# Optimization experiments

Hardware: AMD Instinct MI355X
Metric: run time of the kernel (lower is better)

Reference implementation:

```python
import jax, jax.numpy as jnp
import numpy as np

B, L, C, H, W = 4, 5, 64, 128, 256
VOXEL = 0.4          # args['voxel_size'][0]
DOWNSAMPLE = 2       # args['downsample_rate']


def setup_inputs() -> dict:
    key = jax.random.key(0)
    k1, k2, k3 = jax.random.split(key, 3)
    record_len = jnp.array([3, 5, 4, 4], dtype=jnp.int32)  # sum = 16
    n_tot = 16
    x = jax.random.normal(k1, (n_tot, C, H, W), dtype=jnp.float32)
    # near-identity SE(2)-ish 4x4 transforms so warps stay mostly in-bounds
    eye = jnp.eye(4, dtype=jnp.float32)
    t = jnp.broadcast_to(eye, (B, L, L, 4, 4)).copy()
    rot = jax.random.normal(k2, (B, L, L, 2, 2), dtype=jnp.float32) * 0.02
    trans = jax.random.normal(k3, (B, L, L, 2), dtype=jnp.float32) * 5.0  # meters
    t = t.at[..., :2, :2].add(rot)
    t = t.at[..., 0, 3].set(trans[..., 0])
    t = t.at[..., 1, 3].set(trans[..., 1])
    return {"x": x, "record_len": record_len, "pairwise_t_matrix": t}


def _normalize_t(t):
    # t: (B,L,L,4,4) -> normalized 2x3 affine (matches the torch in-place edits)
    m = t[..., jnp.array([0, 1]), :][..., jnp.array([0, 1, 3])]  # (B,L,L,2,3)
    m = m.at[..., 0, 1].multiply(H / W)
    m = m.at[..., 1, 0].multiply(W / H)
    m = m.at[..., 0, 2].multiply(2.0 / (DOWNSAMPLE * VOXEL * W))
    m = m.at[..., 1, 2].multiply(2.0 / (DOWNSAMPLE * VOXEL * H))
    return m


def _grid_sample(img, grid):
    # img (N,C,H,W), grid (N,H,W,2) xy in [-1,1]; bilinear, zeros padding,
    # align_corners=True (matches torch warp_affine_simple / F.grid_sample)
    n, c, h, w = img.shape
    ix = (grid[..., 0] + 1.0) * 0.5 * (w - 1)
    iy = (grid[..., 1] + 1.0) * 0.5 * (h - 1)
    x0 = jnp.floor(ix); y0 = jnp.floor(iy)
    x1 = x0 + 1.0;      y1 = y0 + 1.0
    wx1 = ix - x0; wx0 = 1.0 - wx1
    wy1 = iy - y0; wy0 = 1.0 - wy1

    def corner(xc, yc, wgt):
        valid = (xc >= 0) & (xc <= w - 1) & (yc >= 0) & (yc <= h - 1)
        xi = jnp.clip(xc, 0, w - 1).astype(jnp.int32)
        yi = jnp.clip(yc, 0, h - 1).astype(jnp.int32)
        vals = jax.vmap(lambda im, yy, xx: im[:, yy, xx])(img, yi, xi)  # (N,C,H,W)
        return vals * (wgt * valid)[:, None, :, :]

    return (corner(x0, y0, wx0 * wy0) + corner(x1, y0, wx1 * wy0)
            + corner(x0, y1, wx0 * wy1) + corner(x1, y1, wx1 * wy1))


def _fuse(x, record_len, pairwise_t_matrix):
    m = _normalize_t(pairwise_t_matrix)          # (B,L,L,2,3)
    theta = m[:, 0]                              # ego row i=0 -> (B,L,2,3)
    # affine_grid, align_corners=True: base grid over [-1,1]
    xs = jnp.linspace(-1.0, 1.0, W)
    ys = jnp.linspace(-1.0, 1.0, H)
    gx, gy = jnp.meshgrid(xs, ys)                # (H,W)
    coords = jnp.stack([gx, gy, jnp.ones_like(gx)], axis=-1)  # (H,W,3)
    grid = jnp.einsum('blij,hwj->blhwi', theta, coords)        # (B,L,H,W,2)
    # pad ragged groups to (B,L,...) via gather
    csum = jnp.cumsum(record_len)
    offsets = jnp.concatenate([jnp.zeros((1,), csum.dtype), csum[:-1]])
    idx = jnp.clip(offsets[:, None] + jnp.arange(L)[None, :], 0, x.shape[0] - 1)
    xp = x[idx]                                  # (B,L,C,H,W)
    warped = _grid_sample(xp.reshape(B * L, C, H, W),
                          grid.reshape(B * L, H, W, 2)).reshape(B, L, C, H, W)
    mask = jnp.arange(L)[None, :] < record_len[:, None]        # (B,L)
    neg_inf = jnp.array(-jnp.inf, dtype=warped.dtype)
    masked = jnp.where(mask[:, :, None, None, None], warped, neg_inf)
    return jnp.max(masked, axis=1)               # (B,C,H,W)


def reference(x, record_len, pairwise_t_matrix):
    return _fuse(x, record_len, pairwise_t_matrix)
```

## Files before the change

### kernel.cpp

```cpp
#include <hip/hip_runtime.h>
#include <math.h>

#define BB 4
#define LL 5
#define CC 64
#define HH 128
#define WW 256
#define NTOT 16
#define CG 8
#define HW (HH * WW)
#define NXCD 8
#define NWG (BB * (CC / CG) * HH)

__global__ __launch_bounds__(256) void maxfusion_kernel(
    const float* __restrict__ x,
    const int* __restrict__ record_len,
    const float* __restrict__ t,
    float* __restrict__ out)
{
    const int bid = (blockIdx.x % NXCD) * (NWG / NXCD) + blockIdx.x / NXCD;

    const int h   = bid % HH;
    const int tmp = bid / HH;
    const int cg  = tmp % (CC / CG);
    const int b   = tmp / (CC / CG);
    const int w   = threadIdx.x;

    const int rl = record_len[b];
    int off = 0;
    #pragma unroll
    for (int i = 0; i < BB; ++i) off += (i < b) ? record_len[i] : 0;

    const float gx = -1.0f + 2.0f * (float)w / (float)(WW - 1);
    const float gy = -1.0f + 2.0f * (float)h / (float)(HH - 1);

    float maxv[CG];
    #pragma unroll
    for (int c = 0; c < CG; ++c) maxv[c] = -INFINITY;

    for (int l = 0; l < rl; ++l) {
        const float* tm = t + (size_t)((b * LL * LL + l) * 16);
        const float m00 = tm[0];
        const float m01 = tm[1] * ((float)HH / (float)WW);
        const float m02 = tm[3] * (2.0f / (0.8f * (float)WW));
        const float m10 = tm[4] * ((float)WW / (float)HH);
        const float m11 = tm[5];
        const float m12 = tm[7] * (2.0f / (0.8f * (float)HH));
        const float sx  = 0.5f * (float)(WW - 1);
        const float sy  = 0.5f * (float)(HH - 1);
        const float a00 = m00 * sx, a01 = m01 * sx, a02 = (m02 + 1.0f) * sx;
        const float a10 = m10 * sy, a11 = m11 * sy, a12 = (m12 + 1.0f) * sy;

        const float ix = a00 * gx + a01 * gy + a02;
        const float iy = a10 * gx + a11 * gy + a12;

        const float x0f = floorf(ix), y0f = floorf(iy);
        const float wx1 = ix - x0f, wx0 = 1.0f - wx1;
        const float wy1 = iy - y0f, wy0 = 1.0f - wy1;
        const int x0 = (int)x0f, y0 = (int)y0f;

        const bool inx = (x0 >= 0) && (x0 <= WW - 2);
        const float wxa = inx ? wx0 : ((x0 == -1)     ? wx1 : 0.0f);
        const float wxb = inx ? wx1 : ((x0 == WW - 1) ? wx0 : 0.0f);
        const float wy0v = ((y0 >= 0)     && (y0 <= HH - 1))     ? wy0 : 0.0f;
        const float wy1v = ((y0 + 1 >= 0) && (y0 + 1 <= HH - 1)) ? wy1 : 0.0f;

        const int k  = min(max(x0, 0), WW - 2);
        const int r0 = min(max(y0,     0), HH - 1);
        const int r1 = min(max(y0 + 1, 0), HH - 1);
        const int off0 = r0 * WW + k;
        const int off1 = r1 * WW + k;

        const int n = min(off + l, NTOT - 1);
        const float* base = x + ((size_t)n * CC + (size_t)cg * CG) * HW;

        #pragma unroll
        for (int c = 0; c < CG; ++c) {
            const float* p = base + (size_t)c * HW;
            const float2 q0 = *reinterpret_cast<const float2*>(p + off0);
            const float2 q1 = *reinterpret_cast<const float2*>(p + off1);
            float t0 = q0.x * wxa + q0.y * wxb;
            float t1 = q1.x * wxa + q1.y * wxb;
            float v  = t0 * wy0v + t1 * wy1v;
            maxv[c] = fmaxf(maxv[c], v);
        }
    }

    float* ob = out + (((size_t)b * CC + (size_t)cg * CG) * HH + h) * WW + w;
    #pragma unroll
    for (int c = 0; c < CG; ++c) {
        __builtin_nontemporal_store(maxv[c], ob + (size_t)c * HW);
    }
}

extern "C" void kernel_launch(void* const* d_in, const int* in_sizes, int n_in,
                              void* d_out, int out_size, void* d_ws, size_t ws_size,
                              hipStream_t stream) {
    const float* x          = (const float*)d_in[0];
    const int*   record_len = (const int*)d_in[1];
    const float* t          = (const float*)d_in[2];
    float* out = (float*)d_out;

    maxfusion_kernel<<<NWG, 256, 0, stream>>>(x, record_len, t, out);
}
```

Measured before the change: 46.58 us.

## Process four output rows per block and reorder block-to-work mapping

Each block now computes four consecutive output rows instead of one, cutting the grid size by four and raising per-thread memory-level parallelism with more independent loads in flight. The XCD-aware block remapping is replaced by a mapping where consecutive block IDs cover different channel groups of the same rows. The launch bounds gain an occupancy hint, and the clamp on the batch index is dropped. Register pressure rises from the larger accumulator array, which may reduce occupancy.

```diff
diff --git a/kernel.cpp b/kernel.cpp
--- a/kernel.cpp
+++ b/kernel.cpp
@@ -8,35 +8,36 @@
 #define WW 256
 #define NTOT 16
 #define CG 8
+#define HB 4
 #define HW (HH * WW)
-#define NXCD 8
-#define NWG (BB * (CC / CG) * HH)
+#define NHB (HH / HB)
+#define NWG (BB * (CC / CG) * NHB)
 
-__global__ __launch_bounds__(256) void maxfusion_kernel(
+__global__ __launch_bounds__(256, 4) void maxfusion_kernel(
     const float* __restrict__ x,
     const int* __restrict__ record_len,
     const float* __restrict__ t,
     float* __restrict__ out)
 {
-    const int bid = (blockIdx.x % NXCD) * (NWG / NXCD) + blockIdx.x / NXCD;
-
-    const int h   = bid % HH;
-    const int tmp = bid / HH;
-    const int cg  = tmp % (CC / CG);
-    const int b   = tmp / (CC / CG);
-    const int w   = threadIdx.x;
+    const int cg = blockIdx.x % 8;
+    const int i  = blockIdx.x / 8;
+    const int b  = i / NHB;
+    const int hb = i % NHB;
+    const int h0 = hb * HB;
+    const int w  = threadIdx.x;
 
     const int rl = record_len[b];
     int off = 0;
     #pragma unroll
-    for (int i = 0; i < BB; ++i) off += (i < b) ? record_len[i] : 0;
+    for (int j = 0; j < BB; ++j) off += (j < b) ? record_len[j] : 0;
 
     const float gx = -1.0f + 2.0f * (float)w / (float)(WW - 1);
-    const float gy = -1.0f + 2.0f * (float)h / (float)(HH - 1);
 
-    float maxv[CG];
+    float maxv[HB][CG];
     #pragma unroll
-    for (int c = 0; c < CG; ++c) maxv[c] = -INFINITY;
+    for (int hh = 0; hh < HB; ++hh)
+        #pragma unroll
+        for (int c = 0; c < CG; ++c) maxv[hh][c] = -INFINITY;
 
     for (int l = 0; l < rl; ++l) {
         const float* tm = t + (size_t)((b * LL * LL + l) * 16);
@@ -51,46 +52,57 @@
         const float a00 = m00 * sx, a01 = m01 * sx, a02 = (m02 + 1.0f) * sx;
         const float a10 = m10 * sy, a11 = m11 * sy, a12 = (m12 + 1.0f) * sy;
 
-        const float ix = a00 * gx + a01 * gy + a02;
-        const float iy = a10 * gx + a11 * gy + a12;
+        float wxa[HB], wxb[HB], wy0v[HB], wy1v[HB];
+        int off0[HB], off1[HB];
+        #pragma unroll
+        for (int hh = 0; hh < HB; ++hh) {
+            const float gy = -1.0f + 2.0f * (float)(h0 + hh) / (float)(HH - 1);
+            const float ix = a00 * gx + a01 * gy + a02;
+            const float iy = a10 * gx + a11 * gy + a12;
 
-        const float x0f = floorf(ix), y0f = floorf(iy);
-        const float wx1 = ix - x0f, wx0 = 1.0f - wx1;
-        const float wy1 = iy - y0f, wy0 = 1.0f - wy1;
-        const int x0 = (int)x0f, y0 = (int)y0f;
+            const float x0f = floorf(ix), y0f = floorf(iy);
+            const float wx1 = ix - x0f, wx0 = 1.0f - wx1;
+            const float wy1 = iy - y0f, wy0 = 1.0f - wy1;
+            const int x0 = (int)x0f, y0 = (int)y0f;
 
-        const bool inx = (x0 >= 0) && (x0 <= WW - 2);
-        const float wxa = inx ? wx0 : ((x0 == -1)     ? wx1 : 0.0f);
-        const float wxb = inx ? wx1 : ((x0 == WW - 1) ? wx0 : 0.0f);
-        const float wy0v = ((y0 >= 0)     && (y0 <= HH - 1))     ? wy0 : 0.0f;
-        const float wy1v = ((y0 + 1 >= 0) && (y0 + 1 <= HH - 1)) ? wy1 : 0.0f;
+            const bool inx = (x0 >= 0) && (x0 <= WW - 2);
+            wxa[hh] = inx ? wx0 : ((x0 == -1)     ? wx1 : 0.0f);
+            wxb[hh] = inx ? wx1 : ((x0 == WW - 1) ? wx0 : 0.0f);
+            wy0v[hh] = ((y0 >= 0)     && (y0 <= HH - 1))     ? wy0 : 0.0f;
+            wy1v[hh] = ((y0 + 1 >= 0) && (y0 + 1 <= HH - 1)) ? wy1 : 0.0f;
 
-        const int k  = min(max(x0, 0), WW - 2);
-        const int r0 = min(max(y0,     0), HH - 1);
-        const int r1 = min(max(y0 + 1, 0), HH - 1);
-        const int off0 = r0 * WW + k;
-        const int off1 = r1 * WW + k;
+            const int k  = min(max(x0, 0), WW - 2);
+            const int r0 = min(max(y0,     0), HH - 1);
+            const int r1 = min(max(y0 + 1, 0), HH - 1);
+            off0[hh] = r0 * WW + k;
+            off1[hh] = r1 * WW + k;
+        }
 
-        const int n = min(off + l, NTOT - 1);
+        const int n = off + l;
         const float* base = x + ((size_t)n * CC + (size_t)cg * CG) * HW;
 
         #pragma unroll
         for (int c = 0; c < CG; ++c) {
             const float* p = base + (size_t)c * HW;
-            const float2 q0 = *reinterpret_cast<const float2*>(p + off0);
-            const float2 q1 = *reinterpret_cast<const float2*>(p + off1);
-            float t0 = q0.x * wxa + q0.y * wxb;
-            float t1 = q1.x * wxa + q1.y * wxb;
-            float v  = t0 * wy0v + t1 * wy1v;
-            maxv[c] = fmaxf(maxv[c], v);
+            #pragma unroll
+            for (int hh = 0; hh < HB; ++hh) {
+                const float2 q0 = *reinterpret_cast<const float2*>(p + off0[hh]);
+                const float2 q1 = *reinterpret_cast<const float2*>(p + off1[hh]);
+                const float t0 = q0.x * wxa[hh] + q0.y * wxb[hh];
+                const float t1 = q1.x * wxa[hh] + q1.y * wxb[hh];
+                const float v  = t0 * wy0v[hh] + t1 * wy1v[hh];
+                maxv[hh][c] = fmaxf(maxv[hh][c], v);
+            }
         }
     }
 
-    float* ob = out + (((size_t)b * CC + (size_t)cg * CG) * HH + h) * WW + w;
+    float* ob = out + (((size_t)b * CC + (size_t)cg * CG) * HH + h0) * WW + w;
     #pragma unroll
-    for (int c = 0; c < CG; ++c) {
-        __builtin_nontemporal_store(maxv[c], ob + (size_t)c * HW);
-    }
+    for (int c = 0; c < CG; ++c)
+        #pragma unroll
+        for (int hh = 0; hh < HB; ++hh)
+            __builtin_nontemporal_store(maxv[hh][c],
+                                        ob + (size_t)c * HW + (size_t)hh * WW);
 }
 
 extern "C" void kernel_launch(void* const* d_in, const int* in_sizes, int n_in,
```

Result: slower. 60.73 us (+30.4%).
